# Performance work log

Hardware: AMD Instinct MI355X
Metric: run time of the kernel (lower is better)

The kernel has to match this reference:

```python
import jax, jax.numpy as jnp
import numpy as np

EPS = 1e-12  # F.normalize eps


def _gather_neighbors(x, idx):
    # x: [B, C, N] node features; idx: [B, N, K] neighbor ids -> [B, C, N, K]
    B, C, N = x.shape
    K = idx.shape[-1]
    flat = idx.reshape(B, N * K)
    g = jax.vmap(lambda f, i: f[:, i])(x, flat)  # [B, C, N*K]
    return g.reshape(B, C, N, K)


def setup_inputs() -> dict:
    key = jax.random.key(0)
    k1, k2, k3, k4, k5 = jax.random.split(key, 5)
    B, C_in, C_out, N, K = 8, 64, 64, 4096, 16
    x = jax.random.normal(k1, (B, C_in, N, 1), dtype=jnp.float32)
    x_0 = jax.random.normal(k2, (B, C_in, N, 1), dtype=jnp.float32)
    edge_index = jax.random.randint(k3, (2, B, N, K), 0, N, dtype=jnp.int64)
    # pre_nn: 1x1 conv C_in -> C_out, no bias; nn: 1x1 conv (C_out+C_in) -> C_out, no bias
    w_pre = jax.random.normal(k4, (C_out, C_in), dtype=jnp.float32) / np.sqrt(C_in)
    w_nn = jax.random.normal(k5, (C_out, C_out + C_in), dtype=jnp.float32) / np.sqrt(C_out + C_in)
    bias = jax.random.normal(jax.random.fold_in(key, 7), (1, C_out, 1, 1), dtype=jnp.float32) * 0.01
    return {"x": x, "x_0": x_0, "w_pre": w_pre, "w_nn": w_nn, "bias": bias, "edge_index": edge_index}


def reference(x, x_0, w_pre, w_nn, bias, edge_index):
    # x: [B, C_in, N, 1]; edge_index: [2, B, N, K]
    xs = x[..., 0]                              # [B, C_in, N]
    x_j = _gather_neighbors(xs, edge_index[0])  # [B, C_in, N, K]
    # pre_nn: 1x1 conv (no bias) + ReLU
    x_j = jax.nn.relu(jnp.einsum('oc,bcnk->bonk', w_pre, x_j))  # [B, C_out, N, K]
    aggr = jnp.max(x_j, axis=-1, keepdims=True)                 # [B, C_out, N, 1]
    cat = jnp.concatenate((x, aggr), axis=1)                    # [B, C_out+C_in, N, 1]
    out = jax.nn.relu(jnp.einsum('oc,bcnk->bonk', w_nn, cat))   # [B, C_out, N, 1]
    out = out + bias
    # F.normalize(out, dim=1): out / max(||out||_2, eps)
    nrm = jnp.sqrt(jnp.sum(out * out, axis=1, keepdims=True))
    out = out / jnp.maximum(nrm, EPS)
    return out
```

## Files before the change

### kernel.cpp

```cpp
#include <hip/hip_runtime.h>
#include <math.h>

#define BB   8
#define CH   64
#define NN   4096
#define KK   16
#define TILE 64
#define NT   1024
#define PP   72
#define CP   136

typedef __attribute__((ext_vector_type(8))) short bf16x8;
typedef __attribute__((ext_vector_type(4))) float f32x4;

__device__ inline unsigned f2bf(float f) {
    union { float f; unsigned u; } v; v.f = f;
    return (v.u + 0x7FFFu + ((v.u >> 16) & 1u)) >> 16;
}

__device__ inline void decode_block(int bi, int& b, int& n0) {
    b = bi & 7; n0 = (bi >> 3) * TILE;
}

__global__ __launch_bounds__(NT, 8) void pre_kernel(
    const float* __restrict__ x,
    const float* __restrict__ w_pre,
    unsigned short* __restrict__ preB)
{
    __shared__ unsigned short xT[TILE * PP];
    __shared__ unsigned short wS[CH * PP];
    const int t    = threadIdx.x;
    const int lane = t & 63;
    const int wv   = __builtin_amdgcn_readfirstlane(t >> 6);
    int b, n0; decode_block(blockIdx.x, b, n0);

    {
        const int c0 = wv * 4;
        unsigned h[4];
#pragma unroll
        for (int p = 0; p < 4; ++p)
            h[p] = f2bf(x[((size_t)b * CH + c0 + p) * NN + n0 + lane]);
        uint2 pk; pk.x = h[0] | (h[1] << 16); pk.y = h[2] | (h[3] << 16);
        *(uint2*)&xT[lane * PP + c0] = pk;
    }
    {
        const int o = t >> 4, c0 = (t & 15) * 4;
        const float4 w = *(const float4*)&w_pre[o * CH + c0];
        uint2 pk; pk.x = f2bf(w.x) | (f2bf(w.y) << 16);
        pk.y = f2bf(w.z) | (f2bf(w.w) << 16);
        *(uint2*)&wS[o * PP + c0] = pk;
    }
    __syncthreads();

    const int mt = wv & 3, nt = wv >> 2, nl = lane & 15, q = lane >> 4;
    const bf16x8 a0 = *(const bf16x8*)&wS[(mt * 16 + nl) * PP + q * 8];
    const bf16x8 a1 = *(const bf16x8*)&wS[(mt * 16 + nl) * PP + 32 + q * 8];
    const bf16x8 b0 = *(const bf16x8*)&xT[(nt * 16 + nl) * PP + q * 8];
    const bf16x8 b1 = *(const bf16x8*)&xT[(nt * 16 + nl) * PP + 32 + q * 8];
    f32x4 acc = {0.f, 0.f, 0.f, 0.f};
    acc = __builtin_amdgcn_mfma_f32_16x16x32_bf16(a0, b0, acc, 0, 0, 0);
    acc = __builtin_amdgcn_mfma_f32_16x16x32_bf16(a1, b1, acc, 0, 0, 0);

    const int n = n0 + nt * 16 + nl;
    unsigned h0 = f2bf(fmaxf(acc[0], 0.f)), h1 = f2bf(fmaxf(acc[1], 0.f));
    unsigned h2 = f2bf(fmaxf(acc[2], 0.f)), h3 = f2bf(fmaxf(acc[3], 0.f));
    uint2 pk; pk.x = h0 | (h1 << 16); pk.y = h2 | (h3 << 16);
    *(uint2*)&preB[((size_t)b * NN + n) * CH + mt * 16 + q * 4] = pk;
}

__global__ __launch_bounds__(NT, 8) void main_kernel(
    const float* __restrict__ x,
    const unsigned short* __restrict__ preB,
    const float* __restrict__ w_nn,
    const float* __restrict__ bias,
    const int* __restrict__ edge0,
    float* __restrict__ out)
{
    __shared__ unsigned short catT[TILE * CP];
    __shared__ unsigned short wS[CH * CP];
    __shared__ float part[TILE][4];
    const int t    = threadIdx.x;
    const int lane = t & 63;
    const int wv   = __builtin_amdgcn_readfirstlane(t >> 6);
    int b, n0; decode_block(blockIdx.x, b, n0);

    const int idxv = edge0[((size_t)b * NN + n0 + wv * 4) * KK + lane];

    {
        const int o = t >> 4, c0 = (t & 15) * 8;
        const float4 wa = *(const float4*)&w_nn[o * 2 * CH + c0];
        const float4 wb = *(const float4*)&w_nn[o * 2 * CH + c0 + 4];
        uint4 pk;
        pk.x = f2bf(wa.x) | (f2bf(wa.y) << 16);
        pk.y = f2bf(wa.z) | (f2bf(wa.w) << 16);
        pk.z = f2bf(wb.x) | (f2bf(wb.y) << 16);
        pk.w = f2bf(wb.z) | (f2bf(wb.w) << 16);
        *(uint4*)&wS[o * CP + c0] = pk;
    }
    {
        const int c0 = wv * 4;
        unsigned h[4];
#pragma unroll
        for (int p = 0; p < 4; ++p)
            h[p] = f2bf(x[((size_t)b * CH + c0 + p) * NN + n0 + lane]);
        uint2 pk; pk.x = h[0] | (h[1] << 16); pk.y = h[2] | (h[3] << 16);
        *(uint2*)&catT[lane * CP + c0] = pk;
    }
    const unsigned short* pb = preB + (size_t)b * NN * CH + lane;
#pragma unroll
    for (int i = 0; i < 4; ++i) {
        unsigned ag = 0;
#pragma unroll
        for (int k = 0; k < KK; ++k) {
            const int nb = __shfl(idxv, i * KK + k, 64) & (NN - 1);
            const unsigned v = pb[(size_t)nb * CH];
            ag = ag > v ? ag : v;
        }
        catT[(wv * 4 + i) * CP + CH + lane] = (unsigned short)ag;
    }
    __syncthreads();

    const int mt = wv & 3, nt = wv >> 2, nl = lane & 15, q = lane >> 4;
    f32x4 acc = {0.f, 0.f, 0.f, 0.f};
#pragma unroll
    for (int kq = 0; kq < 4; ++kq) {
        const bf16x8 af = *(const bf16x8*)&wS[(mt * 16 + nl) * CP + kq * 32 + q * 8];
        const bf16x8 bf = *(const bf16x8*)&catT[(nt * 16 + nl) * CP + kq * 32 + q * 8];
        acc = __builtin_amdgcn_mfma_f32_16x16x32_bf16(af, bf, acc, 0, 0, 0);
    }

    float v[4], ss = 0.f;
#pragma unroll
    for (int r = 0; r < 4; ++r) {
        v[r] = fmaxf(acc[r], 0.f) + bias[mt * 16 + q * 4 + r];
        ss += v[r] * v[r];
    }
    ss += __shfl_xor(ss, 16, 64);
    ss += __shfl_xor(ss, 32, 64);
    if (lane < 16) part[nt * 16 + nl][mt] = ss;
    __syncthreads();
    const float s4 = part[nt * 16 + nl][0] + part[nt * 16 + nl][1]
                   + part[nt * 16 + nl][2] + part[nt * 16 + nl][3];
    const float scale = 1.f / fmaxf(sqrtf(s4), 1e-12f);

    const int n = n0 + nt * 16 + nl;
#pragma unroll
    for (int r = 0; r < 4; ++r)
        out[((size_t)b * CH + mt * 16 + q * 4 + r) * NN + n] = v[r] * scale;
}

extern "C" void kernel_launch(void* const* d_in, const int* in_sizes, int n_in,
                              void* d_out, int out_size, void* d_ws, size_t ws_size,
                              hipStream_t stream) {
    const float* x     = (const float*)d_in[0];
    const float* w_pre = (const float*)d_in[2];
    const float* w_nn  = (const float*)d_in[3];
    const float* bias  = (const float*)d_in[4];
    const int*   edge  = (const int*)d_in[5];

    unsigned short* preB = (unsigned short*)d_ws;
    float* outp = (float*)d_out;

    const dim3 grid(BB * NN / TILE);
    const dim3 block(NT);
    pre_kernel<<<grid, block, 0, stream>>>(x, w_pre, preB);
    main_kernel<<<grid, block, 0, stream>>>(x, preB, w_nn, bias, edge, outp);
}
```

Measured before the change: 88.30 us.

## Fuse pre and main kernels with grid-wide atomic barrier and vectorized gather

Merges the pre-projection kernel and the gather/aggregate kernel into one persistent launch of 256 blocks, each handling two node tiles, separated by a software grid barrier built on an atomic counter. It also reworks the neighbor gather so each lane loads four channels at once and takes a packed 16-bit max, cutting the number of gather loads. The aim is to remove the second kernel launch and to make the gather more efficient. In exchange it adds a zeroing launch, a spin-wait that depends on all 256 blocks being co-resident, and less parallelism per block.

Result: slower. 237.2 us (+168.6%).

```diff
diff --git a/kernel.cpp b/kernel.cpp
--- a/kernel.cpp
+++ b/kernel.cpp
@@ -7,84 +7,62 @@
 #define KK   16
 #define TILE 64
 #define NT   1024
+#define NBLK 256
 #define PP   72
 #define CP   136
+#define CNT_OFF (8u << 20)
 
 typedef __attribute__((ext_vector_type(8))) short bf16x8;
 typedef __attribute__((ext_vector_type(4))) float f32x4;
+typedef __attribute__((ext_vector_type(4))) unsigned short u16x4;
 
 __device__ inline unsigned f2bf(float f) {
     union { float f; unsigned u; } v; v.f = f;
     return (v.u + 0x7FFFu + ((v.u >> 16) & 1u)) >> 16;
 }
 
-__device__ inline void decode_block(int bi, int& b, int& n0) {
-    b = bi & 7; n0 = (bi >> 3) * TILE;
+__device__ inline uint2 pkmax(uint2 a, uint2 b) {
+#if __has_builtin(__builtin_elementwise_max)
+    u16x4 r = __builtin_elementwise_max(*(u16x4*)&a, *(u16x4*)&b);
+    return *(uint2*)&r;
+#else
+    uint2 r;
+    r.x = (((a.x >> 16) > (b.x >> 16)) ? (a.x & 0xFFFF0000u) : (b.x & 0xFFFF0000u))
+        | (((a.x & 0xFFFFu) > (b.x & 0xFFFFu)) ? (a.x & 0xFFFFu) : (b.x & 0xFFFFu));
+    r.y = (((a.y >> 16) > (b.y >> 16)) ? (a.y & 0xFFFF0000u) : (b.y & 0xFFFF0000u))
+        | (((a.y & 0xFFFFu) > (b.y & 0xFFFFu)) ? (a.y & 0xFFFFu) : (b.y & 0xFFFFu));
+    return r;
+#endif
 }
 
-__global__ __launch_bounds__(NT, 8) void pre_kernel(
+__global__ void zero_cnt(unsigned* c) { *c = 0u; }
+
+__global__ __launch_bounds__(NT, 4) void fused_kernel(
     const float* __restrict__ x,
     const float* __restrict__ w_pre,
-    unsigned short* __restrict__ preB)
-{
-    __shared__ unsigned short xT[TILE * PP];
-    __shared__ unsigned short wS[CH * PP];
-    const int t    = threadIdx.x;
-    const int lane = t & 63;
-    const int wv   = __builtin_amdgcn_readfirstlane(t >> 6);
-    int b, n0; decode_block(blockIdx.x, b, n0);
-
-    {
-        const int c0 = wv * 4;
-        unsigned h[4];
-#pragma unroll
-        for (int p = 0; p < 4; ++p)
-            h[p] = f2bf(x[((size_t)b * CH + c0 + p) * NN + n0 + lane]);
-        uint2 pk; pk.x = h[0] | (h[1] << 16); pk.y = h[2] | (h[3] << 16);
-        *(uint2*)&xT[lane * PP + c0] = pk;
-    }
-    {
-        const int o = t >> 4, c0 = (t & 15) * 4;
-        const float4 w = *(const float4*)&w_pre[o * CH + c0];
-        uint2 pk; pk.x = f2bf(w.x) | (f2bf(w.y) << 16);
-        pk.y = f2bf(w.z) | (f2bf(w.w) << 16);
-        *(uint2*)&wS[o * PP + c0] = pk;
-    }
-    __syncthreads();
-
-    const int mt = wv & 3, nt = wv >> 2, nl = lane & 15, q = lane >> 4;
-    const bf16x8 a0 = *(const bf16x8*)&wS[(mt * 16 + nl) * PP + q * 8];
-    const bf16x8 a1 = *(const bf16x8*)&wS[(mt * 16 + nl) * PP + 32 + q * 8];
-    const bf16x8 b0 = *(const bf16x8*)&xT[(nt * 16 + nl) * PP + q * 8];
-    const bf16x8 b1 = *(const bf16x8*)&xT[(nt * 16 + nl) * PP + 32 + q * 8];
-    f32x4 acc = {0.f, 0.f, 0.f, 0.f};
-    acc = __builtin_amdgcn_mfma_f32_16x16x32_bf16(a0, b0, acc, 0, 0, 0);
-    acc = __builtin_amdgcn_mfma_f32_16x16x32_bf16(a1, b1, acc, 0, 0, 0);
-
-    const int n = n0 + nt * 16 + nl;
-    unsigned h0 = f2bf(fmaxf(acc[0], 0.f)), h1 = f2bf(fmaxf(acc[1], 0.f));
-    unsigned h2 = f2bf(fmaxf(acc[2], 0.f)), h3 = f2bf(fmaxf(acc[3], 0.f));
-    uint2 pk; pk.x = h0 | (h1 << 16); pk.y = h2 | (h3 << 16);
-    *(uint2*)&preB[((size_t)b * NN + n) * CH + mt * 16 + q * 4] = pk;
-}
-
-__global__ __launch_bounds__(NT, 8) void main_kernel(
-    const float* __restrict__ x,
-    const unsigned short* __restrict__ preB,
     const float* __restrict__ w_nn,
     const float* __restrict__ bias,
-    const int* __restrict__ edge0,
+    const int*   __restrict__ edge0,
+    unsigned short* __restrict__ preB,
+    unsigned* __restrict__ cnt,
     float* __restrict__ out)
 {
     __shared__ unsigned short catT[TILE * CP];
-    __shared__ unsigned short wS[CH * CP];
+    __shared__ unsigned short wP[CH * PP];
+    __shared__ unsigned short wN[CH * CP];
     __shared__ float part[TILE][4];
     const int t    = threadIdx.x;
     const int lane = t & 63;
     const int wv   = __builtin_amdgcn_readfirstlane(t >> 6);
-    int b, n0; decode_block(blockIdx.x, b, n0);
+    const int b    = blockIdx.x & 7;
+    const int p    = blockIdx.x >> 3;
+    const int mt = wv & 3, nt = wv >> 2, nl = lane & 15, q = lane >> 4;
 
-    const int idxv = edge0[((size_t)b * NN + n0 + wv * 4) * KK + lane];
+    const int idx0 = edge0[((size_t)b * NN + (p * 2 + 0) * TILE + wv * 4) * KK + lane];
+    const int idx1 = edge0[((size_t)b * NN + (p * 2 + 1) * TILE + wv * 4) * KK + lane];
+    float bia[4];
+#pragma unroll
+    for (int r = 0; r < 4; ++r) bia[r] = bias[mt * 16 + q * 4 + r];
 
     {
         const int o = t >> 4, c0 = (t & 15) * 8;
@@ -95,58 +73,108 @@
         pk.y = f2bf(wa.z) | (f2bf(wa.w) << 16);
         pk.z = f2bf(wb.x) | (f2bf(wb.y) << 16);
         pk.w = f2bf(wb.z) | (f2bf(wb.w) << 16);
-        *(uint4*)&wS[o * CP + c0] = pk;
+        *(uint4*)&wN[o * CP + c0] = pk;
     }
     {
-        const int c0 = wv * 4;
-        unsigned h[4];
+        const int o = t >> 4, c0 = (t & 15) * 4;
+        const float4 w = *(const float4*)&w_pre[o * CH + c0];
+        uint2 pk; pk.x = f2bf(w.x) | (f2bf(w.y) << 16);
+        pk.y = f2bf(w.z) | (f2bf(w.w) << 16);
+        *(uint2*)&wP[o * PP + c0] = pk;
+    }
+
 #pragma unroll
-        for (int p = 0; p < 4; ++p)
-            h[p] = f2bf(x[((size_t)b * CH + c0 + p) * NN + n0 + lane]);
-        uint2 pk; pk.x = h[0] | (h[1] << 16); pk.y = h[2] | (h[3] << 16);
-        *(uint2*)&catT[lane * CP + c0] = pk;
+    for (int s = 0; s < 2; ++s) {
+        const int n0 = (p * 2 + s) * TILE;
+        __syncthreads();
+        {
+            const int c0 = wv * 4;
+            unsigned h[4];
+#pragma unroll
+            for (int pp = 0; pp < 4; ++pp)
+                h[pp] = f2bf(x[((size_t)b * CH + c0 + pp) * NN + n0 + lane]);
+            uint2 pk; pk.x = h[0] | (h[1] << 16); pk.y = h[2] | (h[3] << 16);
+            *(uint2*)&catT[lane * CP + c0] = pk;
+        }
+        __syncthreads();
+        const bf16x8 a0 = *(const bf16x8*)&wP[(mt * 16 + nl) * PP + q * 8];
+        const bf16x8 a1 = *(const bf16x8*)&wP[(mt * 16 + nl) * PP + 32 + q * 8];
+        const bf16x8 b0 = *(const bf16x8*)&catT[(nt * 16 + nl) * CP + q * 8];
+        const bf16x8 b1 = *(const bf16x8*)&catT[(nt * 16 + nl) * CP + 32 + q * 8];
+        f32x4 acc = {0.f, 0.f, 0.f, 0.f};
+        acc = __builtin_amdgcn_mfma_f32_16x16x32_bf16(a0, b0, acc, 0, 0, 0);
+        acc = __builtin_amdgcn_mfma_f32_16x16x32_bf16(a1, b1, acc, 0, 0, 0);
+        const int n = n0 + nt * 16 + nl;
+        const unsigned h0 = f2bf(fmaxf(acc[0], 0.f)), h1 = f2bf(fmaxf(acc[1], 0.f));
+        const unsigned h2 = f2bf(fmaxf(acc[2], 0.f)), h3 = f2bf(fmaxf(acc[3], 0.f));
+        uint2 pk; pk.x = h0 | (h1 << 16); pk.y = h2 | (h3 << 16);
+        *(uint2*)&preB[((size_t)b * NN + n) * CH + mt * 16 + q * 4] = pk;
     }
-    const unsigned short* pb = preB + (size_t)b * NN * CH + lane;
-#pragma unroll
-    for (int i = 0; i < 4; ++i) {
-        unsigned ag = 0;
-#pragma unroll
-        for (int k = 0; k < KK; ++k) {
-            const int nb = __shfl(idxv, i * KK + k, 64) & (NN - 1);
-            const unsigned v = pb[(size_t)nb * CH];
-            ag = ag > v ? ag : v;
-        }
-        catT[(wv * 4 + i) * CP + CH + lane] = (unsigned short)ag;
+
+    __threadfence();
+    __syncthreads();
+    if (t == 0) {
+        __hip_atomic_fetch_add(cnt, 1u, __ATOMIC_RELEASE, __HIP_MEMORY_SCOPE_AGENT);
+        while (__hip_atomic_load(cnt, __ATOMIC_ACQUIRE, __HIP_MEMORY_SCOPE_AGENT) < NBLK)
+            __builtin_amdgcn_s_sleep(8);
     }
     __syncthreads();
+    __threadfence();
 
-    const int mt = wv & 3, nt = wv >> 2, nl = lane & 15, q = lane >> 4;
-    f32x4 acc = {0.f, 0.f, 0.f, 0.f};
 #pragma unroll
-    for (int kq = 0; kq < 4; ++kq) {
-        const bf16x8 af = *(const bf16x8*)&wS[(mt * 16 + nl) * CP + kq * 32 + q * 8];
-        const bf16x8 bf = *(const bf16x8*)&catT[(nt * 16 + nl) * CP + kq * 32 + q * 8];
-        acc = __builtin_amdgcn_mfma_f32_16x16x32_bf16(af, bf, acc, 0, 0, 0);
+    for (int s = 0; s < 2; ++s) {
+        const int n0 = (p * 2 + s) * TILE;
+        const int idxv = s ? idx1 : idx0;
+        {
+            const int c0 = wv * 4;
+            unsigned h[4];
+#pragma unroll
+            for (int pp = 0; pp < 4; ++pp)
+                h[pp] = f2bf(x[((size_t)b * CH + c0 + pp) * NN + n0 + lane]);
+            uint2 pk; pk.x = h[0] | (h[1] << 16); pk.y = h[2] | (h[3] << 16);
+            *(uint2*)&catT[lane * CP + c0] = pk;
+        }
+        {
+            const int i = lane >> 4, c0 = (lane & 15) * 4;
+            const unsigned short* pb = preB + (size_t)b * NN * CH + c0;
+            uint2 ag; ag.x = 0u; ag.y = 0u;
+#pragma unroll
+            for (int k = 0; k < KK; ++k) {
+                const int nb = __shfl(idxv, (lane & 48) | k, 64) & (NN - 1);
+                const uint2 v = *(const uint2*)&pb[(size_t)nb * CH];
+                ag = pkmax(ag, v);
+            }
+            *(uint2*)&catT[(wv * 4 + i) * CP + CH + c0] = ag;
+        }
+        __syncthreads();
+
+        f32x4 acc = {0.f, 0.f, 0.f, 0.f};
+#pragma unroll
+        for (int kq = 0; kq < 4; ++kq) {
+            const bf16x8 af = *(const bf16x8*)&wN[(mt * 16 + nl) * CP + kq * 32 + q * 8];
+            const bf16x8 bf = *(const bf16x8*)&catT[(nt * 16 + nl) * CP + kq * 32 + q * 8];
+            acc = __builtin_amdgcn_mfma_f32_16x16x32_bf16(af, bf, acc, 0, 0, 0);
+        }
+
+        float v[4], ss = 0.f;
+#pragma unroll
+        for (int r = 0; r < 4; ++r) {
+            v[r] = fmaxf(acc[r], 0.f) + bia[r];
+            ss += v[r] * v[r];
+        }
+        ss += __shfl_xor(ss, 16, 64);
+        ss += __shfl_xor(ss, 32, 64);
+        if (lane < 16) part[nt * 16 + nl][mt] = ss;
+        __syncthreads();
+        const float s4 = part[nt * 16 + nl][0] + part[nt * 16 + nl][1]
+                       + part[nt * 16 + nl][2] + part[nt * 16 + nl][3];
+        const float scale = 1.f / fmaxf(sqrtf(s4), 1e-12f);
+        const int n = n0 + nt * 16 + nl;
+#pragma unroll
+        for (int r = 0; r < 4; ++r)
+            out[((size_t)b * CH + mt * 16 + q * 4 + r) * NN + n] = v[r] * scale;
+        __syncthreads();
     }
-
-    float v[4], ss = 0.f;
-#pragma unroll
-    for (int r = 0; r < 4; ++r) {
-        v[r] = fmaxf(acc[r], 0.f) + bias[mt * 16 + q * 4 + r];
-        ss += v[r] * v[r];
-    }
-    ss += __shfl_xor(ss, 16, 64);
-    ss += __shfl_xor(ss, 32, 64);
-    if (lane < 16) part[nt * 16 + nl][mt] = ss;
-    __syncthreads();
-    const float s4 = part[nt * 16 + nl][0] + part[nt * 16 + nl][1]
-                   + part[nt * 16 + nl][2] + part[nt * 16 + nl][3];
-    const float scale = 1.f / fmaxf(sqrtf(s4), 1e-12f);
-
-    const int n = n0 + nt * 16 + nl;
-#pragma unroll
-    for (int r = 0; r < 4; ++r)
-        out[((size_t)b * CH + mt * 16 + q * 4 + r) * NN + n] = v[r] * scale;
 }
 
 extern "C" void kernel_launch(void* const* d_in, const int* in_sizes, int n_in,
@@ -159,10 +187,10 @@
     const int*   edge  = (const int*)d_in[5];
 
     unsigned short* preB = (unsigned short*)d_ws;
+    unsigned* cnt = (unsigned*)((char*)d_ws + CNT_OFF);
     float* outp = (float*)d_out;
 
-    const dim3 grid(BB * NN / TILE);
-    const dim3 block(NT);
-    pre_kernel<<<grid, block, 0, stream>>>(x, w_pre, preB);
-    main_kernel<<<grid, block, 0, stream>>>(x, preB, w_nn, bias, edge, outp);
+    zero_cnt<<<1, 1, 0, stream>>>(cnt);
+    fused_kernel<<<dim3(NBLK), dim3(NT), 0, stream>>>(
+        x, w_pre, w_nn, bias, edge, preB, cnt, outp);
 }
```
